# Performance work log

Measured on AMD Instinct MI355X. Metric: run time of the kernel, lower is better.

Reference implementation:

```python
import jax, jax.numpy as jnp
import numpy as np

K = 3  # number_layers

def setup_inputs() -> dict:
    key = jax.random.key(0)
    k1, k2, k3, k4 = jax.random.split(key, 4)
    N, F_in, F_out, E, D = 100000, 256, 64, 1600000, 8
    x = jax.random.normal(k1, (N, F_in), dtype=jnp.float32)
    edge_attr = jax.random.uniform(k2, (E, D), dtype=jnp.float32)
    W = jax.random.normal(k3, (F_in, F_out), dtype=jnp.float32) / np.sqrt(F_in)
    b = jnp.zeros((F_out,), dtype=jnp.float32)
    edge_index = jax.random.randint(k4, (2, E), 0, N, dtype=jnp.int64)
    return {"x": x, "edge_attr": edge_attr, "W": W, "b": b, "edge_index": edge_index}

def reference(x, edge_attr, W, b, edge_index):
    N = x.shape[0]
    # edge_weight from edge_attr
    w = edge_attr.mean(axis=1)  # [E]
    src, dst = edge_index[0], edge_index[1]
    # gcn_norm: add self-loops with weight 1, symmetric normalization
    loop = jnp.arange(N, dtype=edge_index.dtype)
    src_f = jnp.concatenate([src, loop])
    dst_f = jnp.concatenate([dst, loop])
    w_f = jnp.concatenate([w, jnp.ones((N,), dtype=x.dtype)])
    deg = jax.ops.segment_sum(w_f, dst_f, num_segments=N)  # in-degree
    dinv = jnp.where(deg > 0, jax.lax.rsqrt(deg), 0.0)
    norm = dinv[src_f] * w_f * dinv[dst_f]  # [E+N]
    # K hops of x <- A_hat x
    h = x
    for _ in range(K):
        msg = norm[:, None] * h[src_f]              # gather [E+N, F]
        h = jax.ops.segment_sum(msg, dst_f, num_segments=N)  # scatter-add
    out = h @ W + b
    out = jax.nn.relu(out)
    # dropout is a no-op in eval mode
    return jax.nn.log_softmax(out, axis=-1)
```

## Files before the change

kernel.cpp:

```cpp
#include <hip/hip_runtime.h>
#include <hip/hip_bf16.h>


#define F_IN 256
#define F_OUT 64


__global__ __launch_bounds__(256) void init_kernel(int* __restrict__ cnt, int N) {
    int i = blockIdx.x * 256 + threadIdx.x;
    if (i < N) cnt[i] = 0;
}

__global__ __launch_bounds__(256) void edgew_kernel(const float* __restrict__ ea,
                                                    const int* __restrict__ ei,
                                                    int E, int N, float* __restrict__ w,
                                                    int* __restrict__ cnt) {
    int e = blockIdx.x * 256 + threadIdx.x;
    if (e >= E) return;
    const float4* a = (const float4*)(ea + (size_t)e * 8);
    float4 a0 = a[0], a1 = a[1];
    float wv = (a0.x + a0.y + a0.z + a0.w + a1.x + a1.y + a1.z + a1.w) * 0.125f;
    w[e] = wv;
    int d = ei[E + e];
    if ((unsigned)d >= (unsigned)N) return;
    atomicAdd(&cnt[d], 1);
}

__global__ __launch_bounds__(256) void scan1_kernel(const int* __restrict__ cnt, int* __restrict__ ptr,
                                                    int* __restrict__ bsum, int N) {
    __shared__ int s[256];
    int tid = threadIdx.x;
    int base = blockIdx.x * 1024 + tid * 4;
    int c0 = (base + 0 < N) ? cnt[base + 0] : 0;
    int c1 = (base + 1 < N) ? cnt[base + 1] : 0;
    int c2 = (base + 2 < N) ? cnt[base + 2] : 0;
    int c3 = (base + 3 < N) ? cnt[base + 3] : 0;
    int tsum = c0 + c1 + c2 + c3;
    s[tid] = tsum;
    __syncthreads();
    for (int off = 1; off < 256; off <<= 1) {
        int t = (tid >= off) ? s[tid - off] : 0;
        __syncthreads();
        s[tid] += t;
        __syncthreads();
    }
    int excl = s[tid] - tsum;
    if (base + 0 < N) ptr[base + 0] = excl;
    if (base + 1 < N) ptr[base + 1] = excl + c0;
    if (base + 2 < N) ptr[base + 2] = excl + c0 + c1;
    if (base + 3 < N) ptr[base + 3] = excl + c0 + c1 + c2;
    if (tid == 255) bsum[blockIdx.x] = s[255];
}

__global__ __launch_bounds__(256) void scan2_kernel(const int* __restrict__ bsum, int* __restrict__ bscan, int nb) {
    __shared__ int s[256];
    int tid = threadIdx.x;
    int v = (tid < nb) ? bsum[tid] : 0;
    s[tid] = v;
    __syncthreads();
    for (int off = 1; off < 256; off <<= 1) {
        int t = (tid >= off) ? s[tid - off] : 0;
        __syncthreads();
        s[tid] += t;
        __syncthreads();
    }
    if (tid < nb) bscan[tid] = s[tid] - v;
}

__global__ __launch_bounds__(256) void scan3_kernel(int* __restrict__ ptr, const int* __restrict__ bscan,
                                                    int* __restrict__ cursor, int N) {
    int i = blockIdx.x * 256 + threadIdx.x;
    if (i < N) {
        int p = ptr[i] + bscan[i >> 10];
        ptr[i] = p;
        cursor[i] = p;
    }
}

__global__ __launch_bounds__(256) void fill_kernel(const int* __restrict__ ei,
                                                   const float* __restrict__ w,
                                                   int* __restrict__ cursor,
                                                   int2* __restrict__ csr, int E, int N) {
    int e = blockIdx.x * 256 + threadIdx.x;
    if (e >= E) return;
    int s = ei[e];
    int d = ei[E + e];
    if ((unsigned)s >= (unsigned)N || (unsigned)d >= (unsigned)N) return;
    int slot = atomicAdd(&cursor[d], 1);
    csr[slot] = make_int2(s, __float_as_int(w[e]));
}

__global__ __launch_bounds__(256) void degk_kernel(const int* __restrict__ ptr, const int* __restrict__ cnt,
                                                   const int2* __restrict__ csr,
                                                   float* __restrict__ dinv, float* __restrict__ sqrtdeg, int N) {
    int i = blockIdx.x * 256 + threadIdx.x;
    if (i >= N) return;
    int p = ptr[i], c = cnt[i];
    float deg = 1.0f;
    for (int j = 0; j < c; ++j) deg += __int_as_float(csr[p + j].y);
    dinv[i] = rsqrtf(deg);
    sqrtdeg[i] = sqrtf(deg);
}

__global__ __launch_bounds__(256) void xw_kernel(const float* __restrict__ x, const float* __restrict__ W,
                                                 const float* __restrict__ dinv,
                                                 float* __restrict__ y, int N) {
    __shared__ float Wl[F_IN * F_OUT];
    const float4* W4 = (const float4*)W;
    float4* Wl4 = (float4*)Wl;
    for (int i = threadIdx.x; i < F_IN * F_OUT / 4; i += 256) Wl4[i] = W4[i];
    __syncthreads();

    int wave = (blockIdx.x * 256 + threadIdx.x) >> 6;
    int nwaves = (gridDim.x * 256) >> 6;
    int lane = threadIdx.x & 63;
    int r = lane >> 4;
    int jg = lane & 15;
    int ngroups = (N + 3) >> 2;

    for (int g = wave; g < ngroups; g += nwaves) {
        int row = g * 4 + r;
        if (row >= N) continue;
        const float4* xr = (const float4*)(x + (size_t)row * F_IN);
        float ax = 0.f, ay = 0.f, az = 0.f, aw = 0.f;
#pragma unroll 4
        for (int k4 = 0; k4 < F_IN / 4; ++k4) {
            float4 xv = xr[k4];
            float4 w0 = Wl4[(k4 * 4 + 0) * 16 + jg];
            float4 w1 = Wl4[(k4 * 4 + 1) * 16 + jg];
            float4 w2 = Wl4[(k4 * 4 + 2) * 16 + jg];
            float4 w3 = Wl4[(k4 * 4 + 3) * 16 + jg];
            ax = fmaf(xv.x, w0.x, ax); ay = fmaf(xv.x, w0.y, ay); az = fmaf(xv.x, w0.z, az); aw = fmaf(xv.x, w0.w, aw);
            ax = fmaf(xv.y, w1.x, ax); ay = fmaf(xv.y, w1.y, ay); az = fmaf(xv.y, w1.z, az); aw = fmaf(xv.y, w1.w, aw);
            ax = fmaf(xv.z, w2.x, ax); ay = fmaf(xv.z, w2.y, ay); az = fmaf(xv.z, w2.z, az); aw = fmaf(xv.z, w2.w, aw);
            ax = fmaf(xv.w, w3.x, ax); ay = fmaf(xv.w, w3.y, ay); az = fmaf(xv.w, w3.z, az); aw = fmaf(xv.w, w3.w, aw);
        }
        float di = dinv[row];
        float4 acc = {ax * di, ay * di, az * di, aw * di};
        ((float4*)(y + (size_t)row * F_OUT))[jg] = acc;
    }
}

__global__ __launch_bounds__(256) void prop_kernel(const float* __restrict__ gin, float* __restrict__ gout,
                                                   const int* __restrict__ ptr, const int* __restrict__ cnt,
                                                   const float* __restrict__ dinv,
                                                   const int2* __restrict__ csr, int N) {
    int node = blockIdx.x * 4 + (threadIdx.x >> 6);
    if (node >= N) return;
    int lane = threadIdx.x & 63;
    float acc = gin[(size_t)node * 64 + lane];
    int p = ptr[node], c = cnt[node];
    int i = 0;
    for (; i + 4 <= c; i += 4) {
        int2 e0 = csr[p + i + 0];
        int2 e1 = csr[p + i + 1];
        int2 e2 = csr[p + i + 2];
        int2 e3 = csr[p + i + 3];
        float v0 = gin[(size_t)e0.x * 64 + lane];
        float v1 = gin[(size_t)e1.x * 64 + lane];
        float v2 = gin[(size_t)e2.x * 64 + lane];
        float v3 = gin[(size_t)e3.x * 64 + lane];
        acc = fmaf(__int_as_float(e0.y), v0, acc);
        acc = fmaf(__int_as_float(e1.y), v1, acc);
        acc = fmaf(__int_as_float(e2.y), v2, acc);
        acc = fmaf(__int_as_float(e3.y), v3, acc);
    }
    for (; i < c; ++i) {
        int2 e = csr[p + i];
        acc = fmaf(__int_as_float(e.y), gin[(size_t)e.x * 64 + lane], acc);
    }
    float di = dinv[node];
    gout[(size_t)node * 64 + lane] = acc * di * di;
}

__global__ __launch_bounds__(256) void finalize_kernel(float* __restrict__ h, const float* __restrict__ b,
                                                       const float* __restrict__ sqrtdeg, int N) {
    int node = blockIdx.x * 4 + (threadIdx.x >> 6);
    if (node >= N) return;
    int lane = threadIdx.x & 63;
    float v = h[(size_t)node * 64 + lane] * sqrtdeg[node] + b[lane];
    v = fmaxf(v, 0.0f);
    float m = v;
    for (int off = 32; off; off >>= 1) m = fmaxf(m, __shfl_xor(m, off, 64));
    float ex = expf(v - m);
    float s = ex;
    for (int off = 32; off; off >>= 1) s += __shfl_xor(s, off, 64);
    h[(size_t)node * 64 + lane] = (v - m) - logf(s);
}


extern "C" void kernel_launch(void* const* d_in, const int* in_sizes, int n_in,
                              void* d_out, int out_size, void* d_ws, size_t ws_size,
                              hipStream_t stream) {
    const float* x = (const float*)d_in[0];
    const float* edge_attr = (const float*)d_in[1];
    const float* W = (const float*)d_in[2];
    const float* b = (const float*)d_in[3];
    const int* ei = (const int*)d_in[4];
    int N = in_sizes[0] / F_IN;
    int E = in_sizes[4] / 2;
    float* out = (float*)d_out;

    char* ws = (char*)d_ws;
    size_t off = 0;
    auto alloc = [&](size_t bytes) -> char* {
        char* p = ws + off;
        off += (bytes + 255) & ~(size_t)255;
        return p;
    };
    float* dinv    = (float*)alloc((size_t)N * 4);
    float* sqrtdeg = (float*)alloc((size_t)N * 4);
    int*   cnt     = (int*)alloc((size_t)N * 4);
    int*   ptr     = (int*)alloc((size_t)N * 4);
    int*   cursor  = (int*)alloc((size_t)N * 4);
    int*   bsum    = (int*)alloc(256 * 4);
    int*   bscan   = (int*)alloc(256 * 4);
    float* w       = (float*)alloc((size_t)E * 4);
    int2*  csr     = (int2*)alloc((size_t)E * 8);
    float* h0      = (float*)alloc((size_t)N * 64 * 4);

    int nbN = (N + 255) / 256;
    int nbE = (E + 255) / 256;
    int nb1024 = (N + 1023) / 1024;
    int nbNode4 = (N + 3) / 4;

    init_kernel<<<nbN, 256, 0, stream>>>(cnt, N);
    edgew_kernel<<<nbE, 256, 0, stream>>>(edge_attr, ei, E, N, w, cnt);
    scan1_kernel<<<nb1024, 256, 0, stream>>>(cnt, ptr, bsum, N);
    scan2_kernel<<<1, 256, 0, stream>>>(bsum, bscan, nb1024);
    scan3_kernel<<<nbN, 256, 0, stream>>>(ptr, bscan, cursor, N);
    fill_kernel<<<nbE, 256, 0, stream>>>(ei, w, cursor, csr, E, N);
    degk_kernel<<<nbN, 256, 0, stream>>>(ptr, cnt, csr, dinv, sqrtdeg, N);

    xw_kernel<<<1024, 256, 0, stream>>>(x, W, dinv, h0, N);

    prop_kernel<<<nbNode4, 256, 0, stream>>>(h0, out, ptr, cnt, dinv, csr, N);
    prop_kernel<<<nbNode4, 256, 0, stream>>>(out, h0, ptr, cnt, dinv, csr, N);
    prop_kernel<<<nbNode4, 256, 0, stream>>>(h0, out, ptr, cnt, dinv, csr, N);

    finalize_kernel<<<nbNode4, 256, 0, stream>>>(out, b, sqrtdeg, N);
}
```

Measured before the change: 727.6 us.

## Fuse edge weights into CSR fill, retile XW, unroll gathers, fuse final hop

Edge-weight means are now computed inside the CSR fill kernel, so the separate weight array write and read are gone and the histogram only reads destinations. The XW kernel uses 1024-thread blocks and computes four rows per lane group so each shared-memory weight load is reused four times. The propagation gather is unrolled to eight edges for more memory-level parallelism. The last hop is fused with bias, ReLU and log-softmax, removing the sqrtdeg array and one full pass over the output. The cost is higher register pressure in the XW and prop kernels.

```diff
diff --git a/kernel.cpp b/kernel.cpp
--- a/kernel.cpp
+++ b/kernel.cpp
@@ -11,17 +11,11 @@
     if (i < N) cnt[i] = 0;
 }
 
-__global__ __launch_bounds__(256) void edgew_kernel(const float* __restrict__ ea,
-                                                    const int* __restrict__ ei,
-                                                    int E, int N, float* __restrict__ w,
-                                                    int* __restrict__ cnt) {
+__global__ __launch_bounds__(256) void hist_kernel(const int* __restrict__ ei_dst,
+                                                   int E, int N, int* __restrict__ cnt) {
     int e = blockIdx.x * 256 + threadIdx.x;
     if (e >= E) return;
-    const float4* a = (const float4*)(ea + (size_t)e * 8);
-    float4 a0 = a[0], a1 = a[1];
-    float wv = (a0.x + a0.y + a0.z + a0.w + a1.x + a1.y + a1.z + a1.w) * 0.125f;
-    w[e] = wv;
-    int d = ei[E + e];
+    int d = ei_dst[e];
     if ((unsigned)d >= (unsigned)N) return;
     atomicAdd(&cnt[d], 1);
 }
@@ -78,7 +72,7 @@
 }
 
 __global__ __launch_bounds__(256) void fill_kernel(const int* __restrict__ ei,
-                                                   const float* __restrict__ w,
+                                                   const float* __restrict__ ea,
                                                    int* __restrict__ cursor,
                                                    int2* __restrict__ csr, int E, int N) {
     int e = blockIdx.x * 256 + threadIdx.x;
@@ -86,58 +80,97 @@
     int s = ei[e];
     int d = ei[E + e];
     if ((unsigned)s >= (unsigned)N || (unsigned)d >= (unsigned)N) return;
+    const float4* a = (const float4*)(ea + (size_t)e * 8);
+    float4 a0 = a[0], a1 = a[1];
+    float wv = (a0.x + a0.y + a0.z + a0.w + a1.x + a1.y + a1.z + a1.w) * 0.125f;
     int slot = atomicAdd(&cursor[d], 1);
-    csr[slot] = make_int2(s, __float_as_int(w[e]));
+    csr[slot] = make_int2(s, __float_as_int(wv));
 }
 
 __global__ __launch_bounds__(256) void degk_kernel(const int* __restrict__ ptr, const int* __restrict__ cnt,
                                                    const int2* __restrict__ csr,
-                                                   float* __restrict__ dinv, float* __restrict__ sqrtdeg, int N) {
+                                                   float* __restrict__ dinv, int N) {
     int i = blockIdx.x * 256 + threadIdx.x;
     if (i >= N) return;
     int p = ptr[i], c = cnt[i];
     float deg = 1.0f;
     for (int j = 0; j < c; ++j) deg += __int_as_float(csr[p + j].y);
     dinv[i] = rsqrtf(deg);
-    sqrtdeg[i] = sqrtf(deg);
-}
-
-__global__ __launch_bounds__(256) void xw_kernel(const float* __restrict__ x, const float* __restrict__ W,
-                                                 const float* __restrict__ dinv,
-                                                 float* __restrict__ y, int N) {
+}
+
+#define ACC4(A, XV) \
+    A.x = fmaf(XV.x, w0.x, A.x); A.y = fmaf(XV.x, w0.y, A.y); A.z = fmaf(XV.x, w0.z, A.z); A.w = fmaf(XV.x, w0.w, A.w); \
+    A.x = fmaf(XV.y, w1.x, A.x); A.y = fmaf(XV.y, w1.y, A.y); A.z = fmaf(XV.y, w1.z, A.z); A.w = fmaf(XV.y, w1.w, A.w); \
+    A.x = fmaf(XV.z, w2.x, A.x); A.y = fmaf(XV.z, w2.y, A.y); A.z = fmaf(XV.z, w2.z, A.z); A.w = fmaf(XV.z, w2.w, A.w); \
+    A.x = fmaf(XV.w, w3.x, A.x); A.y = fmaf(XV.w, w3.y, A.y); A.z = fmaf(XV.w, w3.z, A.z); A.w = fmaf(XV.w, w3.w, A.w);
+
+__global__ __launch_bounds__(1024) void xw_kernel(const float* __restrict__ x, const float* __restrict__ W,
+                                                  const float* __restrict__ dinv,
+                                                  float* __restrict__ y, int N) {
     __shared__ float Wl[F_IN * F_OUT];
     const float4* W4 = (const float4*)W;
     float4* Wl4 = (float4*)Wl;
-    for (int i = threadIdx.x; i < F_IN * F_OUT / 4; i += 256) Wl4[i] = W4[i];
+    for (int i = threadIdx.x; i < F_IN * F_OUT / 4; i += 1024) Wl4[i] = W4[i];
     __syncthreads();
 
-    int wave = (blockIdx.x * 256 + threadIdx.x) >> 6;
-    int nwaves = (gridDim.x * 256) >> 6;
+    int gwave = (blockIdx.x * 1024 + threadIdx.x) >> 6;
+    int nwaves = (gridDim.x * 1024) >> 6;
     int lane = threadIdx.x & 63;
     int r = lane >> 4;
     int jg = lane & 15;
-    int ngroups = (N + 3) >> 2;
-
-    for (int g = wave; g < ngroups; g += nwaves) {
-        int row = g * 4 + r;
-        if (row >= N) continue;
-        const float4* xr = (const float4*)(x + (size_t)row * F_IN);
-        float ax = 0.f, ay = 0.f, az = 0.f, aw = 0.f;
-#pragma unroll 4
-        for (int k4 = 0; k4 < F_IN / 4; ++k4) {
-            float4 xv = xr[k4];
-            float4 w0 = Wl4[(k4 * 4 + 0) * 16 + jg];
-            float4 w1 = Wl4[(k4 * 4 + 1) * 16 + jg];
-            float4 w2 = Wl4[(k4 * 4 + 2) * 16 + jg];
-            float4 w3 = Wl4[(k4 * 4 + 3) * 16 + jg];
-            ax = fmaf(xv.x, w0.x, ax); ay = fmaf(xv.x, w0.y, ay); az = fmaf(xv.x, w0.z, az); aw = fmaf(xv.x, w0.w, aw);
-            ax = fmaf(xv.y, w1.x, ax); ay = fmaf(xv.y, w1.y, ay); az = fmaf(xv.y, w1.z, az); aw = fmaf(xv.y, w1.w, aw);
-            ax = fmaf(xv.z, w2.x, ax); ay = fmaf(xv.z, w2.y, ay); az = fmaf(xv.z, w2.z, az); aw = fmaf(xv.z, w2.w, aw);
-            ax = fmaf(xv.w, w3.x, ax); ay = fmaf(xv.w, w3.y, ay); az = fmaf(xv.w, w3.z, az); aw = fmaf(xv.w, w3.w, aw);
+    int ngroups = (N + 15) >> 4;
+
+    for (int g = gwave; g < ngroups; g += nwaves) {
+        int row0 = g * 16 + r * 4;
+        float4 a0 = {0,0,0,0}, a1 = {0,0,0,0}, a2 = {0,0,0,0}, a3 = {0,0,0,0};
+        if (row0 + 3 < N) {
+            const float4* xr0 = (const float4*)(x + (size_t)(row0 + 0) * F_IN);
+            const float4* xr1 = (const float4*)(x + (size_t)(row0 + 1) * F_IN);
+            const float4* xr2 = (const float4*)(x + (size_t)(row0 + 2) * F_IN);
+            const float4* xr3 = (const float4*)(x + (size_t)(row0 + 3) * F_IN);
+#pragma unroll 2
+            for (int k4 = 0; k4 < F_IN / 4; ++k4) {
+                float4 xv0 = xr0[k4];
+                float4 xv1 = xr1[k4];
+                float4 xv2 = xr2[k4];
+                float4 xv3 = xr3[k4];
+                float4 w0 = Wl4[(k4 * 4 + 0) * 16 + jg];
+                float4 w1 = Wl4[(k4 * 4 + 1) * 16 + jg];
+                float4 w2 = Wl4[(k4 * 4 + 2) * 16 + jg];
+                float4 w3 = Wl4[(k4 * 4 + 3) * 16 + jg];
+                ACC4(a0, xv0)
+                ACC4(a1, xv1)
+                ACC4(a2, xv2)
+                ACC4(a3, xv3)
+            }
+            float d0 = dinv[row0 + 0], d1 = dinv[row0 + 1], d2 = dinv[row0 + 2], d3 = dinv[row0 + 3];
+            a0.x *= d0; a0.y *= d0; a0.z *= d0; a0.w *= d0;
+            a1.x *= d1; a1.y *= d1; a1.z *= d1; a1.w *= d1;
+            a2.x *= d2; a2.y *= d2; a2.z *= d2; a2.w *= d2;
+            a3.x *= d3; a3.y *= d3; a3.z *= d3; a3.w *= d3;
+            ((float4*)(y + (size_t)(row0 + 0) * F_OUT))[jg] = a0;
+            ((float4*)(y + (size_t)(row0 + 1) * F_OUT))[jg] = a1;
+            ((float4*)(y + (size_t)(row0 + 2) * F_OUT))[jg] = a2;
+            ((float4*)(y + (size_t)(row0 + 3) * F_OUT))[jg] = a3;
+        } else {
+            for (int i4 = 0; i4 < 4; ++i4) {
+                int row = row0 + i4;
+                if (row >= N) break;
+                const float4* xr = (const float4*)(x + (size_t)row * F_IN);
+                float4 a = {0,0,0,0};
+                for (int k4 = 0; k4 < F_IN / 4; ++k4) {
+                    float4 xv = xr[k4];
+                    float4 w0 = Wl4[(k4 * 4 + 0) * 16 + jg];
+                    float4 w1 = Wl4[(k4 * 4 + 1) * 16 + jg];
+                    float4 w2 = Wl4[(k4 * 4 + 2) * 16 + jg];
+                    float4 w3 = Wl4[(k4 * 4 + 3) * 16 + jg];
+                    ACC4(a, xv)
+                }
+                float di = dinv[row];
+                a.x *= di; a.y *= di; a.z *= di; a.w *= di;
+                ((float4*)(y + (size_t)row * F_OUT))[jg] = a;
+            }
         }
-        float di = dinv[row];
-        float4 acc = {ax * di, ay * di, az * di, aw * di};
-        ((float4*)(y + (size_t)row * F_OUT))[jg] = acc;
     }
 }
 
@@ -151,19 +184,31 @@
     float acc = gin[(size_t)node * 64 + lane];
     int p = ptr[node], c = cnt[node];
     int i = 0;
-    for (; i + 4 <= c; i += 4) {
+    for (; i + 8 <= c; i += 8) {
         int2 e0 = csr[p + i + 0];
         int2 e1 = csr[p + i + 1];
         int2 e2 = csr[p + i + 2];
         int2 e3 = csr[p + i + 3];
+        int2 e4 = csr[p + i + 4];
+        int2 e5 = csr[p + i + 5];
+        int2 e6 = csr[p + i + 6];
+        int2 e7 = csr[p + i + 7];
         float v0 = gin[(size_t)e0.x * 64 + lane];
         float v1 = gin[(size_t)e1.x * 64 + lane];
         float v2 = gin[(size_t)e2.x * 64 + lane];
         float v3 = gin[(size_t)e3.x * 64 + lane];
+        float v4 = gin[(size_t)e4.x * 64 + lane];
+        float v5 = gin[(size_t)e5.x * 64 + lane];
+        float v6 = gin[(size_t)e6.x * 64 + lane];
+        float v7 = gin[(size_t)e7.x * 64 + lane];
         acc = fmaf(__int_as_float(e0.y), v0, acc);
         acc = fmaf(__int_as_float(e1.y), v1, acc);
         acc = fmaf(__int_as_float(e2.y), v2, acc);
         acc = fmaf(__int_as_float(e3.y), v3, acc);
+        acc = fmaf(__int_as_float(e4.y), v4, acc);
+        acc = fmaf(__int_as_float(e5.y), v5, acc);
+        acc = fmaf(__int_as_float(e6.y), v6, acc);
+        acc = fmaf(__int_as_float(e7.y), v7, acc);
     }
     for (; i < c; ++i) {
         int2 e = csr[p + i];
@@ -173,19 +218,55 @@
     gout[(size_t)node * 64 + lane] = acc * di * di;
 }
 
-__global__ __launch_bounds__(256) void finalize_kernel(float* __restrict__ h, const float* __restrict__ b,
-                                                       const float* __restrict__ sqrtdeg, int N) {
+__global__ __launch_bounds__(256) void prop_final_kernel(const float* __restrict__ gin, float* __restrict__ out,
+                                                         const int* __restrict__ ptr, const int* __restrict__ cnt,
+                                                         const float* __restrict__ dinv,
+                                                         const int2* __restrict__ csr,
+                                                         const float* __restrict__ b, int N) {
     int node = blockIdx.x * 4 + (threadIdx.x >> 6);
     if (node >= N) return;
     int lane = threadIdx.x & 63;
-    float v = h[(size_t)node * 64 + lane] * sqrtdeg[node] + b[lane];
+    float acc = gin[(size_t)node * 64 + lane];
+    int p = ptr[node], c = cnt[node];
+    int i = 0;
+    for (; i + 8 <= c; i += 8) {
+        int2 e0 = csr[p + i + 0];
+        int2 e1 = csr[p + i + 1];
+        int2 e2 = csr[p + i + 2];
+        int2 e3 = csr[p + i + 3];
+        int2 e4 = csr[p + i + 4];
+        int2 e5 = csr[p + i + 5];
+        int2 e6 = csr[p + i + 6];
+        int2 e7 = csr[p + i + 7];
+        float v0 = gin[(size_t)e0.x * 64 + lane];
+        float v1 = gin[(size_t)e1.x * 64 + lane];
+        float v2 = gin[(size_t)e2.x * 64 + lane];
+        float v3 = gin[(size_t)e3.x * 64 + lane];
+        float v4 = gin[(size_t)e4.x * 64 + lane];
+        float v5 = gin[(size_t)e5.x * 64 + lane];
+        float v6 = gin[(size_t)e6.x * 64 + lane];
+        float v7 = gin[(size_t)e7.x * 64 + lane];
+        acc = fmaf(__int_as_float(e0.y), v0, acc);
+        acc = fmaf(__int_as_float(e1.y), v1, acc);
+        acc = fmaf(__int_as_float(e2.y), v2, acc);
+        acc = fmaf(__int_as_float(e3.y), v3, acc);
+        acc = fmaf(__int_as_float(e4.y), v4, acc);
+        acc = fmaf(__int_as_float(e5.y), v5, acc);
+        acc = fmaf(__int_as_float(e6.y), v6, acc);
+        acc = fmaf(__int_as_float(e7.y), v7, acc);
+    }
+    for (; i < c; ++i) {
+        int2 e = csr[p + i];
+        acc = fmaf(__int_as_float(e.y), gin[(size_t)e.x * 64 + lane], acc);
+    }
+    float v = acc * dinv[node] + b[lane];
     v = fmaxf(v, 0.0f);
     float m = v;
     for (int off = 32; off; off >>= 1) m = fmaxf(m, __shfl_xor(m, off, 64));
     float ex = expf(v - m);
     float s = ex;
     for (int off = 32; off; off >>= 1) s += __shfl_xor(s, off, 64);
-    h[(size_t)node * 64 + lane] = (v - m) - logf(s);
+    out[(size_t)node * 64 + lane] = (v - m) - logf(s);
 }
 
 
@@ -209,15 +290,14 @@
         return p;
     };
     float* dinv    = (float*)alloc((size_t)N * 4);
-    float* sqrtdeg = (float*)alloc((size_t)N * 4);
     int*   cnt     = (int*)alloc((size_t)N * 4);
     int*   ptr     = (int*)alloc((size_t)N * 4);
     int*   cursor  = (int*)alloc((size_t)N * 4);
     int*   bsum    = (int*)alloc(256 * 4);
     int*   bscan   = (int*)alloc(256 * 4);
-    float* w       = (float*)alloc((size_t)E * 4);
     int2*  csr     = (int2*)alloc((size_t)E * 8);
     float* h0      = (float*)alloc((size_t)N * 64 * 4);
+    float* h1      = (float*)alloc((size_t)N * 64 * 4);
 
     int nbN = (N + 255) / 256;
     int nbE = (E + 255) / 256;
@@ -225,18 +305,16 @@
     int nbNode4 = (N + 3) / 4;
 
     init_kernel<<<nbN, 256, 0, stream>>>(cnt, N);
-    edgew_kernel<<<nbE, 256, 0, stream>>>(edge_attr, ei, E, N, w, cnt);
+    hist_kernel<<<nbE, 256, 0, stream>>>(ei + E, E, N, cnt);
     scan1_kernel<<<nb1024, 256, 0, stream>>>(cnt, ptr, bsum, N);
     scan2_kernel<<<1, 256, 0, stream>>>(bsum, bscan, nb1024);
     scan3_kernel<<<nbN, 256, 0, stream>>>(ptr, bscan, cursor, N);
-    fill_kernel<<<nbE, 256, 0, stream>>>(ei, w, cursor, csr, E, N);
-    degk_kernel<<<nbN, 256, 0, stream>>>(ptr, cnt, csr, dinv, sqrtdeg, N);
-
-    xw_kernel<<<1024, 256, 0, stream>>>(x, W, dinv, h0, N);
-
-    prop_kernel<<<nbNode4, 256, 0, stream>>>(h0, out, ptr, cnt, dinv, csr, N);
-    prop_kernel<<<nbNode4, 256, 0, stream>>>(out, h0, ptr, cnt, dinv, csr, N);
-    prop_kernel<<<nbNode4, 256, 0, stream>>>(h0, out, ptr, cnt, dinv, csr, N);
-
-    finalize_kernel<<<nbNode4, 256, 0, stream>>>(out, b, sqrtdeg, N);
-}
+    fill_kernel<<<nbE, 256, 0, stream>>>(ei, edge_attr, cursor, csr, E, N);
+    degk_kernel<<<nbN, 256, 0, stream>>>(ptr, cnt, csr, dinv, N);
+
+    xw_kernel<<<256, 1024, 0, stream>>>(x, W, dinv, h0, N);
+
+    prop_kernel<<<nbNode4, 256, 0, stream>>>(h0, h1, ptr, cnt, dinv, csr, N);
+    prop_kernel<<<nbNode4, 256, 0, stream>>>(h1, h0, ptr, cnt, dinv, csr, N);
+    prop_final_kernel<<<nbNode4, 256, 0, stream>>>(h0, out, ptr, cnt, dinv, csr, b, N);
+}
```

New measurement: 641.9 us. -11.8%, faster.
